# Performance work log

Hardware: AMD Instinct MI355X
Metric: run time of the kernel (lower is better)

The kernel has to match this reference:

```python
import jax, jax.numpy as jnp
import numpy as np
import math

EMBED_DIM = 768
HEADS = 6
HEAD_DIM = EMBED_DIM // HEADS


def setup_inputs() -> dict:
    key = jax.random.key(0)
    ks = jax.random.split(key, 9)
    B, L, D = 4, 2048, EMBED_DIM
    s = 1.0 / math.sqrt(D)
    return {
        "x_input": jax.random.normal(ks[0], (B, L, D), dtype=jnp.float32),
        "Wq": jax.random.normal(ks[1], (D, D), dtype=jnp.float32) * s,
        "bq": jnp.zeros((D,), dtype=jnp.float32),
        "Wk": jax.random.normal(ks[2], (D, D), dtype=jnp.float32) * s,
        "bk": jnp.zeros((D,), dtype=jnp.float32),
        "Wv": jax.random.normal(ks[3], (D, D), dtype=jnp.float32) * s,
        "bv": jnp.zeros((D,), dtype=jnp.float32),
        "Wo": jax.random.normal(ks[4], (D, D), dtype=jnp.float32) * s,
        "bo": jnp.zeros((D,), dtype=jnp.float32),
    }


def reference(x_input, Wq, bq, Wk, bk, Wv, bv, Wo, bo):
    B, L, D = x_input.shape
    # QKV projections
    q = x_input @ Wq + bq
    k = x_input @ Wk + bk
    v = x_input @ Wv + bv
    # [B, L, D] -> [B, H, L, hd]
    def split_heads(t):
        return t.reshape(B, L, HEADS, HEAD_DIM).transpose(0, 2, 1, 3)
    q, k, v = split_heads(q), split_heads(k), split_heads(v)
    # scaled dot-product scores [B, H, L, L]
    scores = jnp.einsum("bhqd,bhkd->bhqk", q, k) / math.sqrt(HEAD_DIM)
    # causal mask: query i attends to keys j <= i
    causal = jnp.tril(jnp.ones((L, L), dtype=bool))
    scores = jnp.where(causal, scores, jnp.finfo(scores.dtype).min)
    attn = jax.nn.softmax(scores, axis=-1)
    out = jnp.einsum("bhqk,bhkd->bhqd", attn, v)  # [B, H, L, hd]
    out = out.transpose(0, 2, 1, 3).reshape(B, L, D)
    # output projection (dropout = identity in eval mode)
    return out @ Wo + bo
```

## Files before the change

kernel.cpp:

```cpp
#include <hip/hip_runtime.h>
#include <hip/hip_bf16.h>
#include <stdint.h>

#define D_EMB 768
#define NHEADS 6
#define HD 128
#define BATCH 4
#define SEQ 2048
#define BH (BATCH*NHEADS)
#define M_ROWS (BATCH*SEQ)

typedef float f32x4 __attribute__((ext_vector_type(4)));
typedef __bf16 bf16x8 __attribute__((ext_vector_type(8)));
typedef short short8 __attribute__((ext_vector_type(8)));

__device__ __forceinline__ short f2bf(float f) {
  union { float f; uint32_t u; } x; x.f = f;
  uint32_t r = x.u + 0x7fffu + ((x.u >> 16) & 1u);
  return (short)(r >> 16);
}
__device__ __forceinline__ uint32_t f2bf_pk(float lo, float hi) {
  return (uint32_t)(uint16_t)f2bf(lo) | ((uint32_t)(uint16_t)f2bf(hi) << 16);
}

__device__ __forceinline__ void gload16(const void* g, void* l) {
  __builtin_amdgcn_global_load_lds(
      (const __attribute__((address_space(1))) unsigned int*)g,
      (__attribute__((address_space(3))) unsigned int*)l, 16, 0, 0);
}

__global__ void cvt_f32_bf16_k(const float* __restrict__ in, short* __restrict__ out, int n4) {
  int i = blockIdx.x * 256 + threadIdx.x;
  if (i >= n4) return;
  float4 v = ((const float4*)in)[i];
  short4 o;
  o.x = f2bf(v.x); o.y = f2bf(v.y); o.z = f2bf(v.z); o.w = f2bf(v.w);
  ((short4*)out)[i] = o;
}

__global__ void transpose_w_k(const float* __restrict__ in, short* __restrict__ out, int R, int C) {
  __shared__ float tile[32][33];
  int c0 = blockIdx.x * 32, r0 = blockIdx.y * 32;
  int tx = threadIdx.x, ty = threadIdx.y;
  #pragma unroll
  for (int i = 0; i < 32; i += 8)
    tile[ty + i][tx] = in[(size_t)(r0 + ty + i) * C + (c0 + tx)];
  __syncthreads();
  #pragma unroll
  for (int i = 0; i < 32; i += 8)
    out[(size_t)(c0 + ty + i) * R + (r0 + tx)] = f2bf(tile[tx][ty + i]);
}

__global__ __launch_bounds__(256) void gemm_bt_k(
    const short* __restrict__ A, const short* __restrict__ BT,
    const float* __restrict__ b0, const float* __restrict__ b1, const float* __restrict__ b2,
    float* __restrict__ Cf, short* __restrict__ Cb, short* __restrict__ Vt,
    int M, int N, int K, int mode)
{
  __shared__ short Als[2][128 * 32];
  __shared__ short Bls[2][128 * 32];
  const int tid = threadIdx.x;
  const int lane = tid & 63;
  const int wave = tid >> 6;
  const int m0 = blockIdx.x * 128;
  const int n0 = blockIdx.y * 128;
  const int wm = (wave & 1) * 64;
  const int wn = (wave >> 1) * 64;
  const int frow = lane & 15;
  const int kk = (lane >> 4) * 8;

  #define G_STAGE(buf, k0)                                                       \
    do {                                                                         \
      _Pragma("unroll")                                                          \
      for (int i = 0; i < 2; ++i) {                                              \
        gload16(&A[(size_t)(m0 + i * 64 + (tid >> 2)) * K + (k0) + (tid & 3) * 8], \
                (char*)Als[buf] + i * 4096 + wave * 1024);                       \
        gload16(&BT[(size_t)(n0 + i * 64 + (tid >> 2)) * K + (k0) + (tid & 3) * 8], \
                (char*)Bls[buf] + i * 4096 + wave * 1024);                       \
      }                                                                          \
    } while (0)

  f32x4 acc[4][4] = {};
  G_STAGE(0, 0);
  __syncthreads();
  int buf = 0;
  for (int k0 = 0; k0 < K; k0 += 32) {
    if (k0 + 32 < K) G_STAGE(buf ^ 1, k0 + 32);
    bf16x8 af[4], bfv[4];
    #pragma unroll
    for (int i = 0; i < 4; ++i) {
      af[i]  = *(const bf16x8*)((const char*)Als[buf] + (wm + i * 16 + frow) * 64 + kk * 2);
      bfv[i] = *(const bf16x8*)((const char*)Bls[buf] + (wn + i * 16 + frow) * 64 + kk * 2);
    }
    #pragma unroll
    for (int i = 0; i < 4; ++i)
      #pragma unroll
      for (int j = 0; j < 4; ++j)
        acc[i][j] = __builtin_amdgcn_mfma_f32_16x16x32_bf16(af[i], bfv[j], acc[i][j], 0, 0, 0);
    __syncthreads();
    buf ^= 1;
  }
  #undef G_STAGE

  const int r0l = (lane >> 4) * 4;
  const int cl = lane & 15;
  const int t3 = n0 / 768;
  const int nloc = n0 - t3 * 768;
  const float* bp = (t3 == 0) ? b0 : ((t3 == 1) ? b1 : b2);
  short* Cbt = Cb + (size_t)t3 * ((size_t)BH * SEQ * HD);
  #pragma unroll
  for (int i = 0; i < 4; ++i) {
    #pragma unroll
    for (int j = 0; j < 4; ++j) {
      int coll = nloc + wn + j * 16 + cl;
      float bv = bp[coll];
      if (mode == 0) {
        #pragma unroll
        for (int r = 0; r < 4; ++r) {
          int m = m0 + wm + i * 16 + r0l + r;
          Cf[(size_t)m * N + (n0 + wn + j * 16 + cl)] = acc[i][j][r] + bv;
        }
      } else if (t3 == 2) {
        int mb = m0 + wm + i * 16 + r0l;
        int b = mb >> 11, li = mb & 2047;
        int h = coll >> 7, d = coll & 127;
        uint2 w;
        w.x = f2bf_pk(acc[i][j][0] + bv, acc[i][j][1] + bv);
        w.y = f2bf_pk(acc[i][j][2] + bv, acc[i][j][3] + bv);
        *(uint2*)&Vt[(((size_t)b * NHEADS + h) * HD + d) * SEQ + li] = w;
      } else {
        #pragma unroll
        for (int r = 0; r < 4; ++r) {
          int m = m0 + wm + i * 16 + r0l + r;
          int b = m >> 11, li = m & 2047;
          int h = coll >> 7, d = coll & 127;
          Cbt[((((size_t)b * NHEADS + h) << 11) + li) * HD + d] = f2bf(acc[i][j][r] + bv);
        }
      }
    }
  }
}

__global__ __launch_bounds__(256, 2) void attn_causal_k(
    const short* __restrict__ Q, const short* __restrict__ K,
    const short* __restrict__ Vt, short* __restrict__ O)
{
  __shared__ __attribute__((aligned(16))) short Kls[2][64 * 128];
  __shared__ __attribute__((aligned(16))) short Vls[2][128 * 64];
  __shared__ __attribute__((aligned(16))) short Pls[4][16 * 64];

  const int tid = threadIdx.x;
  const int lane = tid & 63;
  const int wave = tid >> 6;
  const int g = lane >> 4;
  const int cl = lane & 15;

  const int bid = (int)blockIdx.x;
  const int sid = (bid & 7) * 96 + (bid >> 3);
  const int bh = sid >> 5;
  const int qb = 31 - (sid & 31);
  const int q0 = qb * 64;
  const int qw0 = q0 + wave * 16;

  const short* Qh = Q + (size_t)bh * SEQ * HD;
  const short* Kh = K + (size_t)bh * SEQ * HD;
  const short* Vh = Vt + (size_t)bh * SEQ * HD;

  bf16x8 qf[4];
  #pragma unroll
  for (int c = 0; c < 4; ++c)
    qf[c] = *(const bf16x8*)&Qh[(size_t)(qw0 + cl) * HD + c * 32 + g * 8];

  f32x4 o[8] = {};
  float lrow[4] = {0.f, 0.f, 0.f, 0.f};

  const float kSc = 0.08838834764831845f * 1.44269504088896341f;
  const int swzr = (cl & 7) << 4;
  char* Pw = (char*)&Pls[wave][0];
  const int nt = qb + 1;

  #define STAGE(b, t)                                                            \
    do {                                                                         \
      const int j0s = (t) * 64;                                                  \
      _Pragma("unroll")                                                          \
      for (int i = 0; i < 4; ++i) {                  \
        int row = i * 16 + wave * 4 + (lane >> 4);                               \
        int colb = ((lane & 15) * 16) ^ (((row >> 2) & 7) << 4);                 \
        gload16((const char*)Kh + (size_t)(j0s + row) * 256 + colb,              \
                (char*)Kls[b] + i * 4096 + wave * 1024);                         \
      }                                                                          \
      _Pragma("unroll")                                                          \
      for (int i = 0; i < 4; ++i) {                 \
        int row = i * 32 + wave * 8 + (lane >> 3);                               \
        int colb = ((lane & 7) * 16) ^ ((row & 7) << 4);                         \
        gload16((const char*)Vh + ((size_t)row * SEQ + j0s) * 2 + colb,          \
                (char*)Vls[b] + i * 4096 + wave * 1024);                         \
      }                                                                          \
    } while (0)

  STAGE(0, 0);
  int buf = 0;
  for (int t = 0; t < nt; ++t) {
    __syncthreads();
    if (t + 1 < nt) STAGE(buf ^ 1, t + 1);
    const int j0 = t * 64;

    f32x4 s[4] = {};
    __builtin_amdgcn_s_setprio(1);
    #pragma unroll
    for (int jf = 0; jf < 4; ++jf) {
      const int key = 4 * cl + jf;
      #pragma unroll
      for (int c = 0; c < 4; ++c) {
        bf16x8 kf = *(const bf16x8*)((const char*)Kls[buf] + key * 256 +
                                     ((c * 64 + g * 16) ^ (((key >> 2) & 7) << 4)));
        s[jf] = __builtin_amdgcn_mfma_f32_16x16x32_bf16(qf[c], kf, s[jf], 0, 0, 0);
      }
    }
    __builtin_amdgcn_s_setprio(0);

    #pragma unroll
    for (int r = 0; r < 4; ++r) {
      const int qi = qw0 + g * 4 + r;
      const int rl = g * 4 + r;
      float p[4];
      #pragma unroll
      for (int jf = 0; jf < 4; ++jf) {
        const int j = j0 + 4 * cl + jf;
        p[jf] = (j > qi) ? 0.f : __builtin_amdgcn_exp2f(s[jf][r] * kSc);
      }
      lrow[r] += (p[0] + p[1]) + (p[2] + p[3]);
      uint2 w;
      w.x = f2bf_pk(p[0], p[1]);
      w.y = f2bf_pk(p[2], p[3]);
      *(uint2*)(Pw + rl * 128 + ((cl * 8) ^ ((rl & 7) << 4))) = w;
    }
    asm volatile("s_waitcnt lgkmcnt(0)" ::: "memory");
    __builtin_amdgcn_sched_barrier(0);

    __builtin_amdgcn_s_setprio(1);
    #pragma unroll
    for (int ks = 0; ks < 2; ++ks) {
      bf16x8 pf = *(const bf16x8*)(Pw + cl * 128 + ((ks * 64 + g * 16) ^ swzr));
      #pragma unroll
      for (int f = 0; f < 8; ++f) {
        bf16x8 vf = *(const bf16x8*)((const char*)Vls[buf] + (f * 16 + cl) * 128 +
                                     ((ks * 64 + g * 16) ^ swzr));
        o[f] = __builtin_amdgcn_mfma_f32_16x16x32_bf16(pf, vf, o[f], 0, 0, 0);
      }
    }
    __builtin_amdgcn_s_setprio(0);
    buf ^= 1;
  }
  #undef STAGE

  #pragma unroll
  for (int r = 0; r < 4; ++r)
    #pragma unroll
    for (int off2 = 1; off2 < 16; off2 <<= 1)
      lrow[r] += __shfl_xor(lrow[r], off2);

  const int b = bh / NHEADS, h = bh % NHEADS;
  #pragma unroll
  for (int r = 0; r < 4; ++r) {
    const int qi = qw0 + g * 4 + r;
    const float invl = 1.0f / lrow[r];
    size_t base = ((size_t)b * SEQ + qi) * D_EMB + h * HD;
    #pragma unroll
    for (int f = 0; f < 8; ++f)
      O[base + f * 16 + cl] = f2bf(o[f][r] * invl);
  }
}

extern "C" void kernel_launch(void* const* d_in, const int* in_sizes, int n_in,
                              void* d_out, int out_size, void* d_ws, size_t ws_size,
                              hipStream_t stream) {
  const float* x  = (const float*)d_in[0];
  const float* Wq = (const float*)d_in[1];
  const float* bq = (const float*)d_in[2];
  const float* Wk = (const float*)d_in[3];
  const float* bk = (const float*)d_in[4];
  const float* Wv = (const float*)d_in[5];
  const float* bv = (const float*)d_in[6];
  const float* Wo = (const float*)d_in[7];
  const float* bo = (const float*)d_in[8];
  float* out = (float*)d_out;

  char* ws = (char*)d_ws;
  size_t off = 0;
  auto carve = [&](size_t bytes) {
    char* p = ws + off;
    off += (bytes + 255) & ~(size_t)255;
    return p;
  };
  short* xb     = (short*)carve((size_t)M_ROWS * D_EMB * 2);
  short* wqkvT  = (short*)carve((size_t)3 * D_EMB * D_EMB * 2);
  short* wot    = (short*)carve((size_t)D_EMB * D_EMB * 2);
  short* Qb  = (short*)carve((size_t)BH * SEQ * HD * 2);
  short* Kb  = (short*)carve((size_t)BH * SEQ * HD * 2);
  short* Vtb = (short*)carve((size_t)BH * SEQ * HD * 2);
  short* Ob  = (short*)carve((size_t)M_ROWS * D_EMB * 2);

  int n4 = M_ROWS * D_EMB / 4;
  cvt_f32_bf16_k<<<(n4 + 255) / 256, 256, 0, stream>>>(x, xb, n4);

  dim3 tb(32, 8);
  transpose_w_k<<<dim3(24, 24), tb, 0, stream>>>(Wq, wqkvT,                   D_EMB, D_EMB);
  transpose_w_k<<<dim3(24, 24), tb, 0, stream>>>(Wk, wqkvT +     D_EMB*D_EMB, D_EMB, D_EMB);
  transpose_w_k<<<dim3(24, 24), tb, 0, stream>>>(Wv, wqkvT + 2 * D_EMB*D_EMB, D_EMB, D_EMB);
  transpose_w_k<<<dim3(24, 24), tb, 0, stream>>>(Wo, wot, D_EMB, D_EMB);

  gemm_bt_k<<<dim3(M_ROWS / 128, (3 * D_EMB) / 128), 256, 0, stream>>>(
      xb, wqkvT, bq, bk, bv, nullptr, Qb, Vtb, M_ROWS, 3 * D_EMB, D_EMB, 1);

  attn_causal_k<<<dim3(768), 256, 0, stream>>>(Qb, Kb, Vtb, Ob);

  gemm_bt_k<<<dim3(M_ROWS / 128, D_EMB / 128), 256, 0, stream>>>(
      Ob, wot, bo, bo, bo, out, nullptr, nullptr, M_ROWS, D_EMB, D_EMB, 0);
}
```

Before: 233.5 us.

## Double query rows per attention block and use hardware bf16 pack

```diff
diff --git a/kernel.cpp b/kernel.cpp
--- a/kernel.cpp
+++ b/kernel.cpp
@@ -21,6 +21,11 @@
 }
 __device__ __forceinline__ uint32_t f2bf_pk(float lo, float hi) {
   return (uint32_t)(uint16_t)f2bf(lo) | ((uint32_t)(uint16_t)f2bf(hi) << 16);
+}
+__device__ __forceinline__ uint32_t cvt_pk_bf16(float lo, float hi) {
+  uint32_t r;
+  asm("v_cvt_pk_bf16_f32 %0, %1, %2" : "=v"(r) : "v"(lo), "v"(hi));
+  return r;
 }
 
 __device__ __forceinline__ void gload16(const void* g, void* l) {
@@ -147,7 +152,7 @@
 {
   __shared__ __attribute__((aligned(16))) short Kls[2][64 * 128];
   __shared__ __attribute__((aligned(16))) short Vls[2][128 * 64];
-  __shared__ __attribute__((aligned(16))) short Pls[4][16 * 64];
+  __shared__ __attribute__((aligned(16))) short Pls[4][32 * 64];
 
   const int tid = threadIdx.x;
   const int lane = tid & 63;
@@ -156,28 +161,30 @@
   const int cl = lane & 15;
 
   const int bid = (int)blockIdx.x;
-  const int sid = (bid & 7) * 96 + (bid >> 3);
-  const int bh = sid >> 5;
-  const int qb = 31 - (sid & 31);
-  const int q0 = qb * 64;
-  const int qw0 = q0 + wave * 16;
+  const int sid = (bid & 7) * 48 + (bid >> 3);
+  const int bh = sid >> 4;
+  const int qb = 15 - (sid & 15);
+  const int q0 = qb * 128;
+  const int qw0 = q0 + wave * 32;
 
   const short* Qh = Q + (size_t)bh * SEQ * HD;
   const short* Kh = K + (size_t)bh * SEQ * HD;
   const short* Vh = Vt + (size_t)bh * SEQ * HD;
 
-  bf16x8 qf[4];
-  #pragma unroll
-  for (int c = 0; c < 4; ++c)
-    qf[c] = *(const bf16x8*)&Qh[(size_t)(qw0 + cl) * HD + c * 32 + g * 8];
-
-  f32x4 o[8] = {};
-  float lrow[4] = {0.f, 0.f, 0.f, 0.f};
+  bf16x8 qf[2][4];
+  #pragma unroll
+  for (int m = 0; m < 2; ++m)
+    #pragma unroll
+    for (int c = 0; c < 4; ++c)
+      qf[m][c] = *(const bf16x8*)&Qh[(size_t)(qw0 + m * 16 + cl) * HD + c * 32 + g * 8];
+
+  f32x4 o[2][8] = {};
+  float lrow[2][4] = {};
 
   const float kSc = 0.08838834764831845f * 1.44269504088896341f;
   const int swzr = (cl & 7) << 4;
   char* Pw = (char*)&Pls[wave][0];
-  const int nt = qb + 1;
+  const int nt = 2 * qb + 2;
 
   #define STAGE(b, t)                                                            \
     do {                                                                         \
@@ -205,70 +212,87 @@
     if (t + 1 < nt) STAGE(buf ^ 1, t + 1);
     const int j0 = t * 64;
 
-    f32x4 s[4] = {};
-    __builtin_amdgcn_s_setprio(1);
-    #pragma unroll
-    for (int jf = 0; jf < 4; ++jf) {
-      const int key = 4 * cl + jf;
-      #pragma unroll
-      for (int c = 0; c < 4; ++c) {
-        bf16x8 kf = *(const bf16x8*)((const char*)Kls[buf] + key * 256 +
-                                     ((c * 64 + g * 16) ^ (((key >> 2) & 7) << 4)));
-        s[jf] = __builtin_amdgcn_mfma_f32_16x16x32_bf16(qf[c], kf, s[jf], 0, 0, 0);
+    if (j0 <= qw0 + 31) {
+      f32x4 s[2][4] = {};
+      __builtin_amdgcn_s_setprio(1);
+      #pragma unroll
+      for (int jf = 0; jf < 4; ++jf) {
+        const int key = 4 * cl + jf;
+        #pragma unroll
+        for (int c = 0; c < 4; ++c) {
+          bf16x8 kf = *(const bf16x8*)((const char*)Kls[buf] + key * 256 +
+                                       ((c * 64 + g * 16) ^ ((cl & 7) << 4)));
+          #pragma unroll
+          for (int m = 0; m < 2; ++m)
+            s[m][jf] = __builtin_amdgcn_mfma_f32_16x16x32_bf16(qf[m][c], kf, s[m][jf], 0, 0, 0);
+        }
       }
+      __builtin_amdgcn_s_setprio(0);
+
+      #pragma unroll
+      for (int m = 0; m < 2; ++m) {
+        #pragma unroll
+        for (int r = 0; r < 4; ++r) {
+          const int qi = qw0 + m * 16 + g * 4 + r;
+          const int rl = m * 16 + g * 4 + r;
+          float p[4];
+          #pragma unroll
+          for (int jf = 0; jf < 4; ++jf) {
+            const int j = j0 + 4 * cl + jf;
+            p[jf] = (j > qi) ? 0.f : __builtin_amdgcn_exp2f(s[m][jf][r] * kSc);
+          }
+          lrow[m][r] += (p[0] + p[1]) + (p[2] + p[3]);
+          uint2 w;
+          w.x = cvt_pk_bf16(p[0], p[1]);
+          w.y = cvt_pk_bf16(p[2], p[3]);
+          *(uint2*)(Pw + rl * 128 + ((cl * 8) ^ ((rl & 7) << 4))) = w;
+        }
+      }
+      asm volatile("s_waitcnt lgkmcnt(0)" ::: "memory");
+      __builtin_amdgcn_sched_barrier(0);
+
+      __builtin_amdgcn_s_setprio(1);
+      #pragma unroll
+      for (int ks = 0; ks < 2; ++ks) {
+        bf16x8 pf[2];
+        #pragma unroll
+        for (int m = 0; m < 2; ++m)
+          pf[m] = *(const bf16x8*)(Pw + (m * 16 + cl) * 128 + ((ks * 64 + g * 16) ^ swzr));
+        #pragma unroll
+        for (int f = 0; f < 8; ++f) {
+          bf16x8 vf = *(const bf16x8*)((const char*)Vls[buf] + (f * 16 + cl) * 128 +
+                                       ((ks * 64 + g * 16) ^ swzr));
+          #pragma unroll
+          for (int m = 0; m < 2; ++m)
+            o[m][f] = __builtin_amdgcn_mfma_f32_16x16x32_bf16(pf[m], vf, o[m][f], 0, 0, 0);
+        }
+      }
+      __builtin_amdgcn_s_setprio(0);
     }
-    __builtin_amdgcn_s_setprio(0);
-
-    #pragma unroll
-    for (int r = 0; r < 4; ++r) {
-      const int qi = qw0 + g * 4 + r;
-      const int rl = g * 4 + r;
-      float p[4];
-      #pragma unroll
-      for (int jf = 0; jf < 4; ++jf) {
-        const int j = j0 + 4 * cl + jf;
-        p[jf] = (j > qi) ? 0.f : __builtin_amdgcn_exp2f(s[jf][r] * kSc);
-      }
-      lrow[r] += (p[0] + p[1]) + (p[2] + p[3]);
-      uint2 w;
-      w.x = f2bf_pk(p[0], p[1]);
-      w.y = f2bf_pk(p[2], p[3]);
-      *(uint2*)(Pw + rl * 128 + ((cl * 8) ^ ((rl & 7) << 4))) = w;
-    }
-    asm volatile("s_waitcnt lgkmcnt(0)" ::: "memory");
-    __builtin_amdgcn_sched_barrier(0);
-
-    __builtin_amdgcn_s_setprio(1);
-    #pragma unroll
-    for (int ks = 0; ks < 2; ++ks) {
-      bf16x8 pf = *(const bf16x8*)(Pw + cl * 128 + ((ks * 64 + g * 16) ^ swzr));
-      #pragma unroll
-      for (int f = 0; f < 8; ++f) {
-        bf16x8 vf = *(const bf16x8*)((const char*)Vls[buf] + (f * 16 + cl) * 128 +
-                                     ((ks * 64 + g * 16) ^ swzr));
-        o[f] = __builtin_amdgcn_mfma_f32_16x16x32_bf16(pf, vf, o[f], 0, 0, 0);
-      }
-    }
-    __builtin_amdgcn_s_setprio(0);
     buf ^= 1;
   }
   #undef STAGE
 
   #pragma unroll
-  for (int r = 0; r < 4; ++r)
-    #pragma unroll
-    for (int off2 = 1; off2 < 16; off2 <<= 1)
-      lrow[r] += __shfl_xor(lrow[r], off2);
+  for (int m = 0; m < 2; ++m)
+    #pragma unroll
+    for (int r = 0; r < 4; ++r)
+      #pragma unroll
+      for (int off2 = 1; off2 < 16; off2 <<= 1)
+        lrow[m][r] += __shfl_xor(lrow[m][r], off2);
 
   const int b = bh / NHEADS, h = bh % NHEADS;
   #pragma unroll
-  for (int r = 0; r < 4; ++r) {
-    const int qi = qw0 + g * 4 + r;
-    const float invl = 1.0f / lrow[r];
-    size_t base = ((size_t)b * SEQ + qi) * D_EMB + h * HD;
-    #pragma unroll
-    for (int f = 0; f < 8; ++f)
-      O[base + f * 16 + cl] = f2bf(o[f][r] * invl);
+  for (int m = 0; m < 2; ++m) {
+    #pragma unroll
+    for (int r = 0; r < 4; ++r) {
+      const int qi = qw0 + m * 16 + g * 4 + r;
+      const float invl = 1.0f / lrow[m][r];
+      size_t base = ((size_t)b * SEQ + qi) * D_EMB + h * HD;
+      #pragma unroll
+      for (int f = 0; f < 8; ++f)
+        O[base + f * 16 + cl] = f2bf(o[m][f][r] * invl);
+    }
   }
 }
 
@@ -313,7 +337,7 @@
   gemm_bt_k<<<dim3(M_ROWS / 128, (3 * D_EMB) / 128), 256, 0, stream>>>(
       xb, wqkvT, bq, bk, bv, nullptr, Qb, Vtb, M_ROWS, 3 * D_EMB, D_EMB, 1);
 
-  attn_causal_k<<<dim3(768), 256, 0, stream>>>(Qb, Kb, Vtb, Ob);
+  attn_causal_k<<<dim3(384), 256, 0, stream>>>(Qb, Kb, Vtb, Ob);
 
   gemm_bt_k<<<dim3(M_ROWS / 128, D_EMB / 128), 256, 0, stream>>>(
       Ob, wot, bo, bo, bo, out, nullptr, nullptr, M_ROWS, D_EMB, D_EMB, 0);
```

Measured after the change: 245.0 us. +4.9%, slower.
